# Kernel tuning notes

Measured on AMD Instinct MI355X. Metric: run time of the kernel, lower is better.

Reference implementation:

```python
import jax, jax.numpy as jnp
from jax import lax
import numpy as np

NDIM = 256
BATCH = 65536
NROT = NDIM * (NDIM - 1) // 2  # comb(ndim, 2) = 32640


def _givens_mat(rots, ii, jj, ndim):
    """Product G_last @ ... @ G_1 of Givens rotations in combinations order.

    Left-multiplying by G(i, j, theta) only modifies rows i and j, so we apply
    each rotation as a rank-2 row update instead of a full matmul (same math
    as the original `plane_rot_mat @ mat` loop).
    """
    def step(mat, carry):
        i, j, th = carry
        c = jnp.cos(th)
        s = jnp.sin(th)
        ri = mat[i]
        rj = mat[j]
        mat = mat.at[i].set(c * ri - s * rj)
        mat = mat.at[j].set(s * ri + c * rj)
        return mat, None

    mat0 = jnp.eye(ndim, dtype=jnp.complex64)
    mat, _ = lax.scan(step, mat0, (ii, jj, rots))
    return mat


def setup_inputs() -> dict:
    key = jax.random.key(0)
    k1, k2, k3, k4 = jax.random.split(key, 4)
    x = jax.random.normal(k1, (BATCH, NDIM), dtype=jnp.float32)
    rots1 = 0.1 * jax.random.normal(k2, (NROT,), dtype=jnp.float32)
    phases = 0.1 * jax.random.normal(k3, (NDIM,), dtype=jnp.float32)
    rots2 = 0.1 * jax.random.normal(k4, (NROT,), dtype=jnp.float32)
    return {"x": x, "rots1": rots1, "phases": phases, "rots2": rots2}


def reference(x, rots1, phases, rots2):
    ndim = x.shape[1]
    # np.triu_indices(ndim, 1) enumerates (i, j) pairs in the same row-major
    # order as itertools.combinations(range(ndim), 2).
    ii_np, jj_np = np.triu_indices(ndim, k=1)
    ii = jnp.asarray(ii_np, dtype=jnp.int32)
    jj = jnp.asarray(jj_np, dtype=jnp.int32)

    # vector_norm: row-wise L2 normalization
    xn = x / jnp.linalg.norm(x, axis=1, keepdims=True)
    xc = xn.astype(jnp.complex64)

    # rot1: y = x @ M1.T with M1 = G_last @ ... @ G_1
    M1 = _givens_mat(rots1, ii, jj, ndim)
    y = xc @ M1.T

    # phase_transforms: x @ diag(exp(i*phases)) == elementwise phase multiply
    y = y * jnp.exp(1j * phases)

    # rot2
    M2 = _givens_mat(rots2, ii, jj, ndim)
    y = y @ M2.T

    # measure: |.|^2
    return jnp.abs(y) ** 2
```

## Files before the change

kernel.cpp:

```cpp
#include <hip/hip_runtime.h>
#include <stdint.h>

#define NDIM 256
#define BATCH 65536
#define NROT 32640
#define PBLK 16

typedef float  f32x4 __attribute__((ext_vector_type(4)));
typedef short  s16x8 __attribute__((ext_vector_type(8)));
typedef unsigned int u32x4 __attribute__((ext_vector_type(4)));
typedef unsigned int u32x2 __attribute__((ext_vector_type(2)));

static __device__ __forceinline__ unsigned short f2bf(float f) {
    unsigned int u = __float_as_uint(f);
    u += 0x7fffu + ((u >> 16) & 1u);
    return (unsigned short)(u >> 16);
}

static constexpr size_t OFF_CS   = 0;
static constexpr size_t OFF_PING = 524288;
static constexpr size_t OFF_PONG = OFF_PING + 8388608;
static constexpr size_t OFF_ABT  = OFF_PONG + 8388608;
static constexpr size_t OFF_INV  = OFF_ABT + 262144;
static constexpr size_t OFF_XBF  = OFF_INV + 262144;
static constexpr size_t WS_BIG   = OFF_XBF + (size_t)BATCH * 256 * 2;

__global__ void k_cossin(const float* __restrict__ r1, const float* __restrict__ r2,
                         float2* __restrict__ cs) {
    int i = blockIdx.x * 256 + threadIdx.x;
    if (i < 2 * NROT) {
        float th = (i < NROT) ? r1[i] : r2[i - NROT];
        cs[i] = make_float2(cosf(th), sinf(th));
    }
}

__global__ __launch_bounds__(64) void k_blocks(const float2* __restrict__ cs,
                                               float* __restrict__ bmats) {
    __shared__ float colb[256 * 64];
    __shared__ float2 csb[2304];
    const int t = threadIdx.x;
    const int chunk = blockIdx.x;
    const int b = blockIdx.y;
    const int set = blockIdx.z;
    const int col0 = chunk * 64;

    const int tlo = b * (NROT / PBLK);
    const int thi = (b + 1) * (NROT / PBLK);
    int s0 = -1, s1 = -1, roff = 0, rend = 0;
    {
        int cum = 0;
        for (int i = 0; i <= 255; i++) {
            if (s0 < 0 && cum >= tlo) { s0 = i; roff = cum; }
            if (s1 < 0 && cum >= thi) { s1 = i; rend = cum; }
            cum += 255 - i;
        }
        if (s1 < 0) { s1 = 255; rend = NROT; }
    }
    const int nrot = rend - roff;

    const float2* mycs = cs + (size_t)set * NROT + roff;
    for (int k = t; k < nrot; k += 64) csb[k] = mycs[k];

    {
        const f32x4 z = {0.f, 0.f, 0.f, 0.f};
        #pragma unroll 8
        for (int q = 0; q < 64; q++)
            *(f32x4*)&colb[(q * 64 + t) * 4] = z;
        colb[(col0 + t) * 64 + t] = 1.0f;
    }
    __syncthreads();

    int idx = 0;
    for (int i = s0; i < s1; i++) {
        float u = colb[i * 64 + t];
        const int n = 255 - i;
        const float2* sweep = &csb[idx];
        #pragma unroll 8
        for (int k = 0; k < n; k++) {
            float2 cv = sweep[k];
            float rj = colb[(i + 1 + k) * 64 + t];
            colb[(i + 1 + k) * 64 + t] = cv.y * u + cv.x * rj;
            u = cv.x * u - cv.y * rj;
        }
        idx += n;
        colb[i * 64 + t] = u;
    }

    float* outm = bmats + (size_t)(set * PBLK + b) * 65536;
    for (int r = 0; r < 256; r++)
        outm[(size_t)r * 256 + col0 + t] = colb[r * 64 + t];
}

__global__ __launch_bounds__(256) void k_combine(const float* __restrict__ src,
                                                 float* __restrict__ dst, int half) {
    const int by = blockIdx.y;
    const int set = by / half, pidx = by % half;
    const float* Am = src + (size_t)(set * 2 * half + 2 * pidx + 1) * 65536;
    const float* Bm = src + (size_t)(set * 2 * half + 2 * pidx) * 65536;
    float* Dm = dst + (size_t)(set * half + pidx) * 65536;
    const int tr = blockIdx.x >> 2, tc = blockIdx.x & 3;

    __shared__ float As[64 * 32];
    __shared__ float Bs[32 * 64];
    const int tid = threadIdx.x;
    const int tx = tid & 15, ty = tid >> 4;

    float acc[4][4] = {};
    for (int kb = 0; kb < 8; kb++) {
        __syncthreads();
        #pragma unroll
        for (int it = 0; it < 2; it++) {
            int flat = tid + it * 256;
            int r = flat >> 3, c4 = flat & 7;
            f32x4 v = *(const f32x4*)&Am[(size_t)(tr * 64 + r) * 256 + kb * 32 + c4 * 4];
            *(f32x4*)&As[r * 32 + c4 * 4] = v;
        }
        #pragma unroll
        for (int it = 0; it < 2; it++) {
            int flat = tid + it * 256;
            int r = flat >> 4, c4 = flat & 15;
            f32x4 v = *(const f32x4*)&Bm[(size_t)(kb * 32 + r) * 256 + tc * 64 + c4 * 4];
            *(f32x4*)&Bs[r * 64 + c4 * 4] = v;
        }
        __syncthreads();
        #pragma unroll 8
        for (int kk = 0; kk < 32; kk++) {
            f32x4 bv = *(const f32x4*)&Bs[kk * 64 + tx * 4];
            float a0 = As[(ty * 4 + 0) * 32 + kk];
            float a1 = As[(ty * 4 + 1) * 32 + kk];
            float a2 = As[(ty * 4 + 2) * 32 + kk];
            float a3 = As[(ty * 4 + 3) * 32 + kk];
            #pragma unroll
            for (int j = 0; j < 4; j++) {
                acc[0][j] += a0 * bv[j];
                acc[1][j] += a1 * bv[j];
                acc[2][j] += a2 * bv[j];
                acc[3][j] += a3 * bv[j];
            }
        }
    }
    #pragma unroll
    for (int i = 0; i < 4; i++) {
        f32x4 v = { acc[i][0], acc[i][1], acc[i][2], acc[i][3] };
        *(f32x4*)&Dm[(size_t)(tr * 64 + ty * 4 + i) * 256 + tc * 64 + tx * 4] = v;
    }
}

__global__ __launch_bounds__(256) void k_abt(const float* __restrict__ mats,
                                             const float* __restrict__ phases,
                                             unsigned short* __restrict__ abt) {
    const float* Am = mats + 65536;
    const float* Bm = mats;
    const int v = blockIdx.y;
    const int tr = blockIdx.x >> 2, tc = blockIdx.x & 3;

    __shared__ float As[64 * 32];
    __shared__ float Bs[32 * 64];
    const int tid = threadIdx.x;
    const int tx = tid & 15, ty = tid >> 4;

    float acc[4][4] = {};
    for (int kb = 0; kb < 8; kb++) {
        __syncthreads();
        #pragma unroll
        for (int it = 0; it < 2; it++) {
            int flat = tid + it * 256;
            int r = flat >> 3, c4 = flat & 7;
            f32x4 vv = *(const f32x4*)&Am[(size_t)(tr * 64 + r) * 256 + kb * 32 + c4 * 4];
            *(f32x4*)&As[r * 32 + c4 * 4] = vv;
        }
        #pragma unroll
        for (int it = 0; it < 2; it++) {
            int flat = tid + it * 256;
            int r = flat >> 4, c4 = flat & 15;
            int kg = kb * 32 + r;
            float ph = phases[kg];
            float sc = v ? sinf(ph) : cosf(ph);
            f32x4 vv = *(const f32x4*)&Bm[(size_t)kg * 256 + tc * 64 + c4 * 4];
            vv[0] *= sc; vv[1] *= sc; vv[2] *= sc; vv[3] *= sc;
            *(f32x4*)&Bs[r * 64 + c4 * 4] = vv;
        }
        __syncthreads();
        #pragma unroll 8
        for (int kk = 0; kk < 32; kk++) {
            f32x4 bv = *(const f32x4*)&Bs[kk * 64 + tx * 4];
            float a0 = As[(ty * 4 + 0) * 32 + kk];
            float a1 = As[(ty * 4 + 1) * 32 + kk];
            float a2 = As[(ty * 4 + 2) * 32 + kk];
            float a3 = As[(ty * 4 + 3) * 32 + kk];
            #pragma unroll
            for (int j = 0; j < 4; j++) {
                acc[0][j] += a0 * bv[j];
                acc[1][j] += a1 * bv[j];
                acc[2][j] += a2 * bv[j];
                acc[3][j] += a3 * bv[j];
            }
        }
    }
    #pragma unroll
    for (int i = 0; i < 4; i++) {
        unsigned short h0 = f2bf(acc[i][0]), h1 = f2bf(acc[i][1]);
        unsigned short h2 = f2bf(acc[i][2]), h3 = f2bf(acc[i][3]);
        u32x2 pk = { (unsigned)h0 | ((unsigned)h1 << 16),
                     (unsigned)h2 | ((unsigned)h3 << 16) };
        *(u32x2*)&abt[(size_t)(v * 256 + tr * 64 + ty * 4 + i) * 256 + tc * 64 + tx * 4] = pk;
    }
}

__global__ __launch_bounds__(256) void k_xnorm(const float* __restrict__ x,
                                               unsigned short* __restrict__ xbf) {
    const int row = blockIdx.x * 4 + (threadIdx.x >> 6);
    const int lane = threadIdx.x & 63;
    f32x4 v = *(const f32x4*)&x[(size_t)row * 256 + lane * 4];
    float s = v[0] * v[0] + v[1] * v[1] + v[2] * v[2] + v[3] * v[3];
    for (int off = 32; off; off >>= 1) s += __shfl_xor(s, off, 64);
    float sc = 1.0f / sqrtf(s);
    unsigned short h0 = f2bf(v[0] * sc), h1 = f2bf(v[1] * sc);
    unsigned short h2 = f2bf(v[2] * sc), h3 = f2bf(v[3] * sc);
    u32x2 pk = { (unsigned)h0 | ((unsigned)h1 << 16),
                 (unsigned)h2 | ((unsigned)h3 << 16) };
    *(u32x2*)&xbf[(size_t)row * 256 + lane * 4] = pk;
}

__global__ __launch_bounds__(256) void k_norm(const float* __restrict__ x,
                                              float* __restrict__ invn) {
    const int row = blockIdx.x * 4 + (threadIdx.x >> 6);
    const int lane = threadIdx.x & 63;
    f32x4 v = *(const f32x4*)&x[(size_t)row * 256 + lane * 4];
    float s = v[0] * v[0] + v[1] * v[1] + v[2] * v[2] + v[3] * v[3];
    for (int off = 32; off; off >>= 1) s += __shfl_xor(s, off, 64);
    if (lane == 0) invn[row] = 1.0f / sqrtf(s);
}

#define BKP 136
__global__ __launch_bounds__(256) void k_gemm_bf(const unsigned short* __restrict__ xbf,
                                                 const unsigned short* __restrict__ abt,
                                                 float* __restrict__ out) {
    __shared__ unsigned short As[128 * BKP];
    __shared__ unsigned short Bs[128 * BKP];
    const int tid = threadIdx.x;
    const int cb = blockIdx.x;
    const int rb = blockIdx.y;
    const int lane = tid & 63, w = tid >> 6;

    f32x4 acc[16];
    #pragma unroll
    for (int i = 0; i < 16; i++) acc[i] = (f32x4){0.f, 0.f, 0.f, 0.f};

    for (int kb = 0; kb < 2; kb++) {
        __syncthreads();
        #pragma unroll
        for (int it = 0; it < 8; it++) {
            int flat = tid + it * 256;
            int r = flat >> 4, c8 = flat & 15;
            u32x4 vv = *(const u32x4*)&xbf[(size_t)(rb * 128 + r) * 256 + kb * 128 + c8 * 8];
            *(u32x4*)&As[r * BKP + c8 * 8] = vv;
        }
        #pragma unroll
        for (int it = 0; it < 8; it++) {
            int flat = tid + it * 256;
            int r = flat >> 4, c8 = flat & 15;
            int gr = (r < 64) ? (cb * 64 + r) : (256 + cb * 64 + (r - 64));
            u32x4 vv = *(const u32x4*)&abt[(size_t)gr * 256 + kb * 128 + c8 * 8];
            *(u32x4*)&Bs[r * BKP + c8 * 8] = vv;
        }
        __syncthreads();
        #pragma unroll
        for (int ks = 0; ks < 4; ks++) {
            const int k0 = ks * 32 + (lane >> 4) * 8;
            s16x8 a[2], b[8];
            #pragma unroll
            for (int tm = 0; tm < 2; tm++)
                a[tm] = *(const s16x8*)&As[(w * 32 + tm * 16 + (lane & 15)) * BKP + k0];
            #pragma unroll
            for (int tn = 0; tn < 8; tn++)
                b[tn] = *(const s16x8*)&Bs[(tn * 16 + (lane & 15)) * BKP + k0];
            #pragma unroll
            for (int tm = 0; tm < 2; tm++)
                #pragma unroll
                for (int tn = 0; tn < 8; tn++)
                    acc[tm * 8 + tn] = __builtin_amdgcn_mfma_f32_16x16x32_bf16(
                        a[tm], b[tn], acc[tm * 8 + tn], 0, 0, 0);
        }
    }

    const int qr = lane >> 4, c = lane & 15;
    #pragma unroll
    for (int tm = 0; tm < 2; tm++) {
        #pragma unroll
        for (int tn = 0; tn < 4; tn++) {
            f32x4 p = acc[tm * 8 + tn];
            f32x4 q = acc[tm * 8 + tn + 4];
            #pragma unroll
            for (int r = 0; r < 4; r++) {
                int m = w * 32 + tm * 16 + qr * 4 + r;
                out[(size_t)(rb * 128 + m) * 256 + cb * 64 + tn * 16 + c] =
                    p[r] * p[r] + q[r] * q[r];
            }
        }
    }
}

__global__ __launch_bounds__(256) void k_gemm_f32(const float* __restrict__ x,
                                                  const unsigned short* __restrict__ abt,
                                                  const float* __restrict__ invn,
                                                  float* __restrict__ out) {
    __shared__ unsigned short As[128 * BKP];
    __shared__ unsigned short Bs[128 * BKP];
    const int tid = threadIdx.x;
    const int cb = blockIdx.x;
    const int rb = blockIdx.y;
    const int lane = tid & 63, w = tid >> 6;

    f32x4 acc[16];
    #pragma unroll
    for (int i = 0; i < 16; i++) acc[i] = (f32x4){0.f, 0.f, 0.f, 0.f};

    for (int kb = 0; kb < 2; kb++) {
        __syncthreads();
        #pragma unroll
        for (int it = 0; it < 16; it++) {
            int flat = tid + it * 256;
            int r = flat >> 5, c4 = flat & 31;
            f32x4 v = *(const f32x4*)&x[(size_t)(rb * 128 + r) * 256 + kb * 128 + c4 * 4];
            float sc = invn[rb * 128 + r];
            v[0] *= sc; v[1] *= sc; v[2] *= sc; v[3] *= sc;
            unsigned short h0 = f2bf(v[0]), h1 = f2bf(v[1]);
            unsigned short h2 = f2bf(v[2]), h3 = f2bf(v[3]);
            u32x2 pk = { (unsigned)h0 | ((unsigned)h1 << 16),
                         (unsigned)h2 | ((unsigned)h3 << 16) };
            *(u32x2*)&As[r * BKP + c4 * 4] = pk;
        }
        #pragma unroll
        for (int it = 0; it < 8; it++) {
            int flat = tid + it * 256;
            int r = flat >> 4, c8 = flat & 15;
            int gr = (r < 64) ? (cb * 64 + r) : (256 + cb * 64 + (r - 64));
            u32x4 vv = *(const u32x4*)&abt[(size_t)gr * 256 + kb * 128 + c8 * 8];
            *(u32x4*)&Bs[r * BKP + c8 * 8] = vv;
        }
        __syncthreads();
        #pragma unroll
        for (int ks = 0; ks < 4; ks++) {
            const int k0 = ks * 32 + (lane >> 4) * 8;
            s16x8 a[2], b[8];
            #pragma unroll
            for (int tm = 0; tm < 2; tm++)
                a[tm] = *(const s16x8*)&As[(w * 32 + tm * 16 + (lane & 15)) * BKP + k0];
            #pragma unroll
            for (int tn = 0; tn < 8; tn++)
                b[tn] = *(const s16x8*)&Bs[(tn * 16 + (lane & 15)) * BKP + k0];
            #pragma unroll
            for (int tm = 0; tm < 2; tm++)
                #pragma unroll
                for (int tn = 0; tn < 8; tn++)
                    acc[tm * 8 + tn] = __builtin_amdgcn_mfma_f32_16x16x32_bf16(
                        a[tm], b[tn], acc[tm * 8 + tn], 0, 0, 0);
        }
    }

    const int qr = lane >> 4, c = lane & 15;
    #pragma unroll
    for (int tm = 0; tm < 2; tm++) {
        #pragma unroll
        for (int tn = 0; tn < 4; tn++) {
            f32x4 p = acc[tm * 8 + tn];
            f32x4 q = acc[tm * 8 + tn + 4];
            #pragma unroll
            for (int r = 0; r < 4; r++) {
                int m = w * 32 + tm * 16 + qr * 4 + r;
                out[(size_t)(rb * 128 + m) * 256 + cb * 64 + tn * 16 + c] =
                    p[r] * p[r] + q[r] * q[r];
            }
        }
    }
}

extern "C" void kernel_launch(void* const* d_in, const int* in_sizes, int n_in,
                              void* d_out, int out_size, void* d_ws, size_t ws_size,
                              hipStream_t stream) {
    (void)in_sizes; (void)n_in; (void)out_size;
    const float* x      = (const float*)d_in[0];
    const float* rots1  = (const float*)d_in[1];
    const float* phases = (const float*)d_in[2];
    const float* rots2  = (const float*)d_in[3];
    float* out = (float*)d_out;
    char* ws = (char*)d_ws;

    float2*         cs    = (float2*)(ws + OFF_CS);
    float*          ping  = (float*)(ws + OFF_PING);
    float*          pong  = (float*)(ws + OFF_PONG);
    unsigned short* abt   = (unsigned short*)(ws + OFF_ABT);
    float*          invn  = (float*)(ws + OFF_INV);
    unsigned short* xbf   = (unsigned short*)(ws + OFF_XBF);

    k_cossin<<<(2 * NROT + 255) / 256, 256, 0, stream>>>(rots1, rots2, cs);
    k_blocks<<<dim3(4, PBLK, 2), 64, 0, stream>>>(cs, ping);
    k_combine<<<dim3(16, 16), 256, 0, stream>>>(ping, pong, 8);
    k_combine<<<dim3(16, 8),  256, 0, stream>>>(pong, ping, 4);
    k_combine<<<dim3(16, 4),  256, 0, stream>>>(ping, pong, 2);
    k_combine<<<dim3(16, 2),  256, 0, stream>>>(pong, ping, 1);
    k_abt<<<dim3(16, 2), 256, 0, stream>>>(ping, phases, abt);

    if (ws_size >= WS_BIG) {
        k_xnorm<<<BATCH / 4, 256, 0, stream>>>(x, xbf);
        k_gemm_bf<<<dim3(4, BATCH / 128), 256, 0, stream>>>(xbf, abt, out);
    } else {
        k_norm<<<BATCH / 4, 256, 0, stream>>>(x, invn);
        k_gemm_f32<<<dim3(4, BATCH / 128), 256, 0, stream>>>(x, abt, invn, out);
    }
}
```

Measured before the change: 326.8 us.

## Register-block Givens sweeps four rows at a time and swap GEMM grid order

The rotation-block kernel now processes four consecutive sweeps together, holding the four pivot rows in registers and streaming each other row once through them. This cuts LDS traffic by about four times and drops the shared cos/sin staging in favour of scalar (readfirstlane) global loads. Block boundaries are rounded to multiples of four sweeps, which changes how rotations are split across blocks while keeping their order. Both GEMM launches now put row blocks on grid x and column blocks on y, so the four column blocks that share the same x rows no longer run back to back, which changes cache locality.

```diff
diff --git a/kernel.cpp b/kernel.cpp
--- a/kernel.cpp
+++ b/kernel.cpp
@@ -37,7 +37,6 @@
 __global__ __launch_bounds__(64) void k_blocks(const float2* __restrict__ cs,
                                                float* __restrict__ bmats) {
     __shared__ float colb[256 * 64];
-    __shared__ float2 csb[2304];
     const int t = threadIdx.x;
     const int chunk = blockIdx.x;
     const int b = blockIdx.y;
@@ -46,20 +45,12 @@
 
     const int tlo = b * (NROT / PBLK);
     const int thi = (b + 1) * (NROT / PBLK);
-    int s0 = -1, s1 = -1, roff = 0, rend = 0;
-    {
-        int cum = 0;
-        for (int i = 0; i <= 255; i++) {
-            if (s0 < 0 && cum >= tlo) { s0 = i; roff = cum; }
-            if (s1 < 0 && cum >= thi) { s1 = i; rend = cum; }
-            cum += 255 - i;
-        }
-        if (s1 < 0) { s1 = 255; rend = NROT; }
-    }
-    const int nrot = rend - roff;
-
-    const float2* mycs = cs + (size_t)set * NROT + roff;
-    for (int k = t; k < nrot; k += 64) csb[k] = mycs[k];
+    int s0 = -1, s1 = -1;
+    for (int i = 0; i <= 256; i += 4) {
+        int basei = i * 255 - (i * (i - 1)) / 2;
+        if (s0 < 0 && basei >= tlo) s0 = i;
+        if (s1 < 0 && basei >= thi) s1 = i;
+    }
 
     {
         const f32x4 z = {0.f, 0.f, 0.f, 0.f};
@@ -70,20 +61,82 @@
     }
     __syncthreads();
 
-    int idx = 0;
-    for (int i = s0; i < s1; i++) {
-        float u = colb[i * 64 + t];
-        const int n = 255 - i;
-        const float2* sweep = &csb[idx];
-        #pragma unroll 8
-        for (int k = 0; k < n; k++) {
-            float2 cv = sweep[k];
-            float rj = colb[(i + 1 + k) * 64 + t];
-            colb[(i + 1 + k) * 64 + t] = cv.y * u + cv.x * rj;
-            u = cv.x * u - cv.y * rj;
-        }
-        idx += n;
-        colb[i * 64 + t] = u;
+    const int csoff = set * NROT;
+    for (int g = (s0 >> 2); g < (s1 >> 2); g++) {
+        const int m0 = g * 4;
+        int off[4];
+        #pragma unroll
+        for (int a = 0; a < 4; a++) {
+            int m = m0 + a;
+            int base = m * 255 - (m * (m - 1)) / 2;
+            off[a] = csoff + base - m - 1;
+        }
+        float u[4];
+        #pragma unroll
+        for (int a = 0; a < 4; a++) u[a] = colb[(m0 + a) * 64 + t];
+
+        #pragma unroll
+        for (int a = 0; a < 3; a++) {
+            #pragma unroll
+            for (int bb = a + 1; bb < 4; bb++) {
+                float2 cv = cs[__builtin_amdgcn_readfirstlane(off[a] + m0 + bb)];
+                float nr = cv.y * u[a] + cv.x * u[bb];
+                u[a] = cv.x * u[a] - cv.y * u[bb];
+                u[bb] = nr;
+            }
+        }
+
+        const int jbeg = m0 + 4;
+        float rjbuf[8];
+        #pragma unroll
+        for (int p = 0; p < 8; p++) {
+            int jj = jbeg + p; jj = (jj < 255) ? jj : 255;
+            rjbuf[p] = colb[jj * 64 + t];
+        }
+        int j = jbeg;
+        for (; j + 16 <= 256; j += 8) {
+            #pragma unroll
+            for (int p = 0; p < 8; p++) {
+                float r = rjbuf[p];
+                rjbuf[p] = colb[(j + p + 8) * 64 + t];
+                #pragma unroll
+                for (int a = 0; a < 4; a++) {
+                    float2 cv = cs[__builtin_amdgcn_readfirstlane(off[a] + j + p)];
+                    float nr = cv.y * u[a] + cv.x * r;
+                    u[a] = cv.x * u[a] - cv.y * r;
+                    r = nr;
+                }
+                colb[(j + p) * 64 + t] = r;
+            }
+        }
+        #pragma unroll
+        for (int p = 0; p < 8; p++) {
+            if (j + p < 256) {
+                float r = rjbuf[p];
+                #pragma unroll
+                for (int a = 0; a < 4; a++) {
+                    float2 cv = cs[__builtin_amdgcn_readfirstlane(off[a] + j + p)];
+                    float nr = cv.y * u[a] + cv.x * r;
+                    u[a] = cv.x * u[a] - cv.y * r;
+                    r = nr;
+                }
+                colb[(j + p) * 64 + t] = r;
+            }
+        }
+        j += 8;
+        for (; j < 256; j++) {
+            float r = colb[j * 64 + t];
+            #pragma unroll
+            for (int a = 0; a < 4; a++) {
+                float2 cv = cs[__builtin_amdgcn_readfirstlane(off[a] + j)];
+                float nr = cv.y * u[a] + cv.x * r;
+                u[a] = cv.x * u[a] - cv.y * r;
+                r = nr;
+            }
+            colb[j * 64 + t] = r;
+        }
+        #pragma unroll
+        for (int a = 0; a < 4; a++) colb[(m0 + a) * 64 + t] = u[a];
     }
 
     float* outm = bmats + (size_t)(set * PBLK + b) * 65536;
@@ -239,8 +292,8 @@
     __shared__ unsigned short As[128 * BKP];
     __shared__ unsigned short Bs[128 * BKP];
     const int tid = threadIdx.x;
-    const int cb = blockIdx.x;
-    const int rb = blockIdx.y;
+    const int rb = blockIdx.x;
+    const int cb = blockIdx.y;
     const int lane = tid & 63, w = tid >> 6;
 
     f32x4 acc[16];
@@ -308,8 +361,8 @@
     __shared__ unsigned short As[128 * BKP];
     __shared__ unsigned short Bs[128 * BKP];
     const int tid = threadIdx.x;
-    const int cb = blockIdx.x;
-    const int rb = blockIdx.y;
+    const int rb = blockIdx.x;
+    const int cb = blockIdx.y;
     const int lane = tid & 63, w = tid >> 6;
 
     f32x4 acc[16];
@@ -404,9 +457,9 @@
 
     if (ws_size >= WS_BIG) {
         k_xnorm<<<BATCH / 4, 256, 0, stream>>>(x, xbf);
-        k_gemm_bf<<<dim3(4, BATCH / 128), 256, 0, stream>>>(xbf, abt, out);
+        k_gemm_bf<<<dim3(BATCH / 128, 4), 256, 0, stream>>>(xbf, abt, out);
     } else {
         k_norm<<<BATCH / 4, 256, 0, stream>>>(x, invn);
-        k_gemm_f32<<<dim3(4, BATCH / 128), 256, 0, stream>>>(x, abt, invn, out);
-    }
-}
+        k_gemm_f32<<<dim3(BATCH / 128, 4), 256, 0, stream>>>(x, abt, invn, out);
+    }
+}
```

New measurement: 390.5 us. +19.5%, slower.

## Split Givens chain into more blocks with 4-row grouped sweeps, reorder GEMM grid

Applied to the files above, without the earlier changes.

The rotation sequence is now split into up to 64 independent blocks (chosen at runtime from workspace size) instead of 16, which gives the serial Givens stage more parallel work but adds levels to the combine tree. Each block's sweep now processes four pivot rows at once: the small 4x4 triangle of rotations is applied in registers, then a single pass over the trailing rows applies four rotations per row with prefetched loads. This cuts shared-memory row traffic and loop overhead. The GEMM grid is transposed so consecutive blocks walk the batch dimension, which changes cache locality for the shared weight tile. The risks are more matrix-combine work and larger workspace use.

```diff
diff --git a/kernel.cpp b/kernel.cpp
--- a/kernel.cpp
+++ b/kernel.cpp
@@ -4,7 +4,6 @@
 #define NDIM 256
 #define BATCH 65536
 #define NROT 32640
-#define PBLK 16
 
 typedef float  f32x4 __attribute__((ext_vector_type(4)));
 typedef short  s16x8 __attribute__((ext_vector_type(8)));
@@ -16,14 +15,6 @@
     u += 0x7fffu + ((u >> 16) & 1u);
     return (unsigned short)(u >> 16);
 }
-
-static constexpr size_t OFF_CS   = 0;
-static constexpr size_t OFF_PING = 524288;
-static constexpr size_t OFF_PONG = OFF_PING + 8388608;
-static constexpr size_t OFF_ABT  = OFF_PONG + 8388608;
-static constexpr size_t OFF_INV  = OFF_ABT + 262144;
-static constexpr size_t OFF_XBF  = OFF_INV + 262144;
-static constexpr size_t WS_BIG   = OFF_XBF + (size_t)BATCH * 256 * 2;
 
 __global__ void k_cossin(const float* __restrict__ r1, const float* __restrict__ r2,
                          float2* __restrict__ cs) {
@@ -35,58 +26,111 @@
 }
 
 __global__ __launch_bounds__(64) void k_blocks(const float2* __restrict__ cs,
-                                               float* __restrict__ bmats) {
-    __shared__ float colb[256 * 64];
-    __shared__ float2 csb[2304];
+                                               float* __restrict__ bmats, int pblk) {
+    __shared__ float colb[264 * 64];
+    __shared__ float2 csb[256 * 4];
+    __shared__ float2 tri[20 * 6];
     const int t = threadIdx.x;
     const int chunk = blockIdx.x;
     const int b = blockIdx.y;
     const int set = blockIdx.z;
     const int col0 = chunk * 64;
-
-    const int tlo = b * (NROT / PBLK);
-    const int thi = (b + 1) * (NROT / PBLK);
-    int s0 = -1, s1 = -1, roff = 0, rend = 0;
-    {
-        int cum = 0;
-        for (int i = 0; i <= 255; i++) {
-            if (s0 < 0 && cum >= tlo) { s0 = i; roff = cum; }
-            if (s1 < 0 && cum >= thi) { s1 = i; rend = cum; }
-            cum += 255 - i;
-        }
-        if (s1 < 0) { s1 = 255; rend = NROT; }
-    }
-    const int nrot = rend - roff;
-
-    const float2* mycs = cs + (size_t)set * NROT + roff;
-    for (int k = t; k < nrot; k += 64) csb[k] = mycs[k];
+    const int csoff = set * NROT;
+
+    const int target = NROT / pblk;
+    const int tlo = b * target;
+    const int thi = (b + 1) * target;
+    int s0 = -1, s1 = -1;
+    for (int i = 0; i <= 256; i += 4) {
+        int pre = i * 255 - (i * (i - 1)) / 2;
+        if (s0 < 0 && pre >= tlo) s0 = i;
+        if (s1 < 0 && pre >= thi) s1 = i;
+    }
+    const int ngroups = (s1 - s0) >> 2;
 
     {
         const f32x4 z = {0.f, 0.f, 0.f, 0.f};
-        #pragma unroll 8
-        for (int q = 0; q < 64; q++)
+        #pragma unroll 11
+        for (int q = 0; q < 66; q++)
             *(f32x4*)&colb[(q * 64 + t) * 4] = z;
         colb[(col0 + t) * 64 + t] = 1.0f;
     }
-    __syncthreads();
-
-    int idx = 0;
-    for (int i = s0; i < s1; i++) {
-        float u = colb[i * 64 + t];
-        const int n = 255 - i;
-        const float2* sweep = &csb[idx];
-        #pragma unroll 8
-        for (int k = 0; k < n; k++) {
-            float2 cv = sweep[k];
-            float rj = colb[(i + 1 + k) * 64 + t];
-            colb[(i + 1 + k) * 64 + t] = cv.y * u + cv.x * rj;
-            u = cv.x * u - cv.y * rj;
-        }
-        idx += n;
-        colb[i * 64 + t] = u;
-    }
-
-    float* outm = bmats + (size_t)(set * PBLK + b) * 65536;
+
+    for (int k = t; k < ngroups * 6; k += 64) {
+        int g = k / 6, q = k - g * 6;
+        int a  = (q < 3) ? 0 : ((q < 5) ? 1 : 2);
+        int bb = (q < 3) ? (q + 1) : ((q < 5) ? (q - 1) : 3);
+        int m0 = s0 + g * 4;
+        int m = m0 + a;
+        int base = m * 255 - (m * (m - 1)) / 2;
+        tri[k] = cs[csoff + base - m - 1 + (m0 + bb)];
+    }
+
+    for (int g = 0; g < ngroups; g++) {
+        const int m0 = s0 + g * 4;
+        int off[4];
+        #pragma unroll
+        for (int a = 0; a < 4; a++) {
+            int m = m0 + a;
+            int base = m * 255 - (m * (m - 1)) / 2;
+            off[a] = csoff + base - m - 1;
+        }
+        const int n_j = 252 - m0;
+        const int n_p = (n_j > 0) ? ((n_j + 7) & ~7) : 0;
+
+        for (int k = t; k < n_p * 4; k += 64) {
+            int jj = k >> 2, a = k & 3;
+            int j = m0 + 4 + jj;
+            csb[k] = (j < 256) ? cs[off[a] + j] : make_float2(1.f, 0.f);
+        }
+
+        float u0 = colb[(m0 + 0) * 64 + t];
+        float u1 = colb[(m0 + 1) * 64 + t];
+        float u2 = colb[(m0 + 2) * 64 + t];
+        float u3 = colb[(m0 + 3) * 64 + t];
+
+        {
+            float2 cv; float nr;
+            cv = tri[g * 6 + 0]; nr = cv.y * u0 + cv.x * u1; u0 = cv.x * u0 - cv.y * u1; u1 = nr;
+            cv = tri[g * 6 + 1]; nr = cv.y * u0 + cv.x * u2; u0 = cv.x * u0 - cv.y * u2; u2 = nr;
+            cv = tri[g * 6 + 2]; nr = cv.y * u0 + cv.x * u3; u0 = cv.x * u0 - cv.y * u3; u3 = nr;
+            cv = tri[g * 6 + 3]; nr = cv.y * u1 + cv.x * u2; u1 = cv.x * u1 - cv.y * u2; u2 = nr;
+            cv = tri[g * 6 + 4]; nr = cv.y * u1 + cv.x * u3; u1 = cv.x * u1 - cv.y * u3; u3 = nr;
+            cv = tri[g * 6 + 5]; nr = cv.y * u2 + cv.x * u3; u2 = cv.x * u2 - cv.y * u3; u3 = nr;
+        }
+
+        if (n_p > 0) {
+            float rbuf[8];
+            #pragma unroll
+            for (int p = 0; p < 8; p++)
+                rbuf[p] = colb[(m0 + 4 + p) * 64 + t];
+            for (int c = 0; c < n_p; c += 8) {
+                #pragma unroll
+                for (int p = 0; p < 8; p++) {
+                    const int j = m0 + 4 + c + p;
+                    float r = rbuf[p];
+                    int jn = j + 8; jn = (jn < 263) ? jn : 263;
+                    rbuf[p] = colb[jn * 64 + t];
+                    float2 a0 = csb[(c + p) * 4 + 0];
+                    float2 a1 = csb[(c + p) * 4 + 1];
+                    float2 a2 = csb[(c + p) * 4 + 2];
+                    float2 a3 = csb[(c + p) * 4 + 3];
+                    float nr;
+                    nr = a0.y * u0 + a0.x * r; u0 = a0.x * u0 - a0.y * r; r = nr;
+                    nr = a1.y * u1 + a1.x * r; u1 = a1.x * u1 - a1.y * r; r = nr;
+                    nr = a2.y * u2 + a2.x * r; u2 = a2.x * u2 - a2.y * r; r = nr;
+                    nr = a3.y * u3 + a3.x * r; u3 = a3.x * u3 - a3.y * r; r = nr;
+                    colb[j * 64 + t] = r;
+                }
+            }
+        }
+        colb[(m0 + 0) * 64 + t] = u0;
+        colb[(m0 + 1) * 64 + t] = u1;
+        colb[(m0 + 2) * 64 + t] = u2;
+        colb[(m0 + 3) * 64 + t] = u3;
+    }
+
+    float* outm = bmats + (size_t)(set * pblk + b) * 65536;
     for (int r = 0; r < 256; r++)
         outm[(size_t)r * 256 + col0 + t] = colb[r * 64 + t];
 }
@@ -239,8 +283,8 @@
     __shared__ unsigned short As[128 * BKP];
     __shared__ unsigned short Bs[128 * BKP];
     const int tid = threadIdx.x;
-    const int cb = blockIdx.x;
-    const int rb = blockIdx.y;
+    const int rb = blockIdx.x;
+    const int cb = blockIdx.y;
     const int lane = tid & 63, w = tid >> 6;
 
     f32x4 acc[16];
@@ -308,8 +352,8 @@
     __shared__ unsigned short As[128 * BKP];
     __shared__ unsigned short Bs[128 * BKP];
     const int tid = threadIdx.x;
-    const int cb = blockIdx.x;
-    const int rb = blockIdx.y;
+    const int rb = blockIdx.x;
+    const int cb = blockIdx.y;
     const int lane = tid & 63, w = tid >> 6;
 
     f32x4 acc[16];
@@ -387,26 +431,40 @@
     float* out = (float*)d_out;
     char* ws = (char*)d_ws;
 
-    float2*         cs    = (float2*)(ws + OFF_CS);
-    float*          ping  = (float*)(ws + OFF_PING);
-    float*          pong  = (float*)(ws + OFF_PONG);
-    unsigned short* abt   = (unsigned short*)(ws + OFF_ABT);
-    float*          invn  = (float*)(ws + OFF_INV);
-    unsigned short* xbf   = (unsigned short*)(ws + OFF_XBF);
+    const size_t MAT = 262144;
+    int pblk = 64;
+    while (pblk > 16 &&
+           524288 + (size_t)3 * pblk * MAT + 2 * MAT + (size_t)BATCH * 512 > ws_size)
+        pblk >>= 1;
+    const size_t offA   = 524288;
+    const size_t offB   = offA + (size_t)2 * pblk * MAT;
+    const size_t offABT = offB + (size_t)pblk * MAT;
+    const size_t offINV = offABT + MAT;
+    const size_t offXBF = offINV + MAT;
+    const bool use_xbf = (offXBF + (size_t)BATCH * 512) <= ws_size;
+
+    float2*         cs   = (float2*)(ws);
+    float*          A    = (float*)(ws + offA);
+    float*          B    = (float*)(ws + offB);
+    unsigned short* abt  = (unsigned short*)(ws + offABT);
+    float*          invn = (float*)(ws + offINV);
+    unsigned short* xbf  = (unsigned short*)(ws + offXBF);
 
     k_cossin<<<(2 * NROT + 255) / 256, 256, 0, stream>>>(rots1, rots2, cs);
-    k_blocks<<<dim3(4, PBLK, 2), 64, 0, stream>>>(cs, ping);
-    k_combine<<<dim3(16, 16), 256, 0, stream>>>(ping, pong, 8);
-    k_combine<<<dim3(16, 8),  256, 0, stream>>>(pong, ping, 4);
-    k_combine<<<dim3(16, 4),  256, 0, stream>>>(ping, pong, 2);
-    k_combine<<<dim3(16, 2),  256, 0, stream>>>(pong, ping, 1);
-    k_abt<<<dim3(16, 2), 256, 0, stream>>>(ping, phases, abt);
-
-    if (ws_size >= WS_BIG) {
+    k_blocks<<<dim3(4, pblk, 2), 64, 0, stream>>>(cs, A, pblk);
+
+    float* srcp = A; float* dstp = B;
+    for (int half = pblk / 2; half >= 1; half >>= 1) {
+        k_combine<<<dim3(16, 2 * half), 256, 0, stream>>>(srcp, dstp, half);
+        float* tmp = srcp; srcp = dstp; dstp = tmp;
+    }
+    k_abt<<<dim3(16, 2), 256, 0, stream>>>(srcp, phases, abt);
+
+    if (use_xbf) {
         k_xnorm<<<BATCH / 4, 256, 0, stream>>>(x, xbf);
-        k_gemm_bf<<<dim3(4, BATCH / 128), 256, 0, stream>>>(xbf, abt, out);
+        k_gemm_bf<<<dim3(BATCH / 128, 4), 256, 0, stream>>>(xbf, abt, out);
     } else {
         k_norm<<<BATCH / 4, 256, 0, stream>>>(x, invn);
-        k_gemm_f32<<<dim3(4, BATCH / 128), 256, 0, stream>>>(x, abt, invn, out);
-    }
-}
+        k_gemm_f32<<<dim3(BATCH / 128, 4), 256, 0, stream>>>(x, abt, invn, out);
+    }
+}
```

After: 340.3 us. 4.1% more time.
